# Kernel optimization log

Measured on AMD Instinct MI355X. Metric: run time of the kernel, lower is better.

## Reference

```python
import jax, jax.numpy as jnp
import numpy as np

DIM = 256
NUM_HEADS = 4
HEAD_DIM = DIM // NUM_HEADS


def _linear_params(k, d_in, d_out):
    kw, kb = jax.random.split(k)
    lim = 1.0 / np.sqrt(d_in)
    W = jax.random.uniform(kw, (d_out, d_in), jnp.float32, -lim, lim)
    b = jax.random.uniform(kb, (d_out,), jnp.float32, -lim, lim)
    return W, b


def setup_inputs() -> dict:
    key = jax.random.key(0)
    ks = jax.random.split(key, 10)
    B, Nq, Nkv = 8, 4096, 256
    inp = {
        'node_emb': jax.random.normal(ks[0], (B, Nq, DIM), jnp.float32),
        'cluster_emb': jax.random.normal(ks[1], (B, Nkv, DIM), jnp.float32),
        'clustering_weights': jax.random.normal(ks[2], (B, Nq, Nkv), jnp.float32),
        'ln_q_g': jnp.ones((DIM,), jnp.float32), 'ln_q_b': jnp.zeros((DIM,), jnp.float32),
        'ln_kv_g': jnp.ones((DIM,), jnp.float32), 'ln_kv_b': jnp.zeros((DIM,), jnp.float32),
        'ln_out_g': jnp.ones((DIM,), jnp.float32), 'ln_out_b': jnp.zeros((DIM,), jnp.float32),
    }
    for name, k in [('q', ks[3]), ('k', ks[4]), ('v', ks[5]), ('o', ks[6])]:
        W, b = _linear_params(k, DIM, DIM)
        inp[f'W_{name}'], inp[f'b_{name}'] = W, b
    W1, b1 = _linear_params(ks[7], DIM, DIM)
    W2, b2 = _linear_params(ks[8], DIM, DIM)
    inp.update(W_m1=W1, b_m1=b1, W_m2=W2, b_m2=b2)
    return inp


def _layer_norm(x, g, b, eps=1e-5):
    mu = jnp.mean(x, axis=-1, keepdims=True)
    var = jnp.var(x, axis=-1, keepdims=True)
    return (x - mu) * jax.lax.rsqrt(var + eps) * g + b


def reference(node_emb, cluster_emb, clustering_weights,
              ln_q_g, ln_q_b, ln_kv_g, ln_kv_b, ln_out_g, ln_out_b,
              W_q, b_q, W_k, b_k, W_v, b_v, W_o, b_o,
              W_m1, b_m1, W_m2, b_m2):
    B, Nq, D = node_emb.shape
    Nkv = cluster_emb.shape[1]
    q_in = _layer_norm(node_emb, ln_q_g, ln_q_b)
    kv_in = _layer_norm(cluster_emb, ln_kv_g, ln_kv_b)
    # projections -> [B, H, N, hd]
    Q = (q_in @ W_q.T + b_q).reshape(B, Nq, NUM_HEADS, HEAD_DIM).transpose(0, 2, 1, 3)
    K = (kv_in @ W_k.T + b_k).reshape(B, Nkv, NUM_HEADS, HEAD_DIM).transpose(0, 2, 1, 3)
    V = (kv_in @ W_v.T + b_v).reshape(B, Nkv, NUM_HEADS, HEAD_DIM).transpose(0, 2, 1, 3)
    scores = jnp.einsum('bhqd,bhkd->bhqk', Q, K) / np.sqrt(HEAD_DIM)
    scores = scores + clustering_weights[:, None, :, :]
    attn = jax.nn.softmax(scores, axis=-1)
    ctx = jnp.einsum('bhqk,bhkd->bhqd', attn, V)
    ctx = ctx.transpose(0, 2, 1, 3).reshape(B, Nq, D)
    attn_out = ctx @ W_o.T + b_o
    x = node_emb + attn_out
    h = _layer_norm(x, ln_out_g, ln_out_b)
    h = jax.nn.gelu(h @ W_m1.T + b_m1, approximate=False) @ W_m2.T + b_m2
    out = x + h
    attn_matrix = attn.mean(axis=1)
    return out, attn_matrix
```

## Files before the change

kernel.cpp:

```cpp
#include <hip/hip_runtime.h>
#include <math.h>

typedef __attribute__((ext_vector_type(8))) short short8;
typedef __attribute__((ext_vector_type(4))) float f32x4;
typedef __attribute__((ext_vector_type(2))) unsigned int u32x2;

#define AS1 __attribute__((address_space(1)))
#define AS3 __attribute__((address_space(3)))

__device__ __forceinline__ float b2f(short s){
  return __uint_as_float(((unsigned int)(unsigned short)s) << 16);
}
__device__ __forceinline__ short f2b(float f){
  unsigned int u = __float_as_uint(f);
  u = (u + 0x7fffu + ((u >> 16) & 1u)) >> 16;
  return (short)u;
}
__device__ __forceinline__ unsigned pk2(float lo, float hi){
  return ((unsigned)(unsigned short)f2b(hi) << 16) | (unsigned)(unsigned short)f2b(lo);
}
__device__ __forceinline__ float ulo(unsigned u){ return __uint_as_float(u << 16); }
__device__ __forceinline__ float uhi(unsigned u){ return __uint_as_float(u & 0xffff0000u); }

__global__ __launch_bounds__(256) void cvt_w(
    const float* __restrict__ s0, const float* __restrict__ s1,
    const float* __restrict__ s2, const float* __restrict__ s3,
    const float* __restrict__ s4, const float* __restrict__ s5,
    short* __restrict__ dst, short* __restrict__ dstS)
{
  const float* srcs[6] = {s0, s1, s2, s3, s4, s5};
  int i = blockIdx.x * 256 + threadIdx.x;
  int mat = i >> 16, rc = i & 65535;
  short v = f2b(srcs[mat][rc]);
  dst[i] = v;
  if (mat >= 3){
    int row = rc >> 8, col = rc & 255;
    int d2 = (mat - 3) * 65536 + ((col >> 5) << 13) + (row << 5)
           + (((col >> 3) & 3) << 3) + (col & 7);
    dstS[d2] = v;
  }
}

__global__ __launch_bounds__(256) void ln_k(
    const float* __restrict__ x, const float* __restrict__ g,
    const float* __restrict__ bta, short* __restrict__ y)
{
  const int row = blockIdx.x, t = threadIdx.x;
  const size_t base = (size_t)row * 256;
  float v = x[base + t];
  float s1 = v, s2 = v * v;
  #pragma unroll
  for (int off = 32; off; off >>= 1){ s1 += __shfl_down(s1, off); s2 += __shfl_down(s2, off); }
  __shared__ float a1[4], a2[4];
  __shared__ float mu_s, rs_s;
  if ((t & 63) == 0){ a1[t >> 6] = s1; a2[t >> 6] = s2; }
  __syncthreads();
  if (t == 0){
    float S1 = a1[0] + a1[1] + a1[2] + a1[3];
    float S2 = a2[0] + a2[1] + a2[2] + a2[3];
    float mu = S1 * 0.00390625f;
    float var = S2 * 0.00390625f - mu * mu;
    mu_s = mu; rs_s = rsqrtf(var + 1e-5f);
  }
  __syncthreads();
  y[base + t] = f2b((v - mu_s) * rs_s * g[t] + bta[t]);
}

template<int OT, int LNA>
__global__ __launch_bounds__(256, 2) void gemmW(
    const short* __restrict__ A, const float* __restrict__ Af,
    const short* __restrict__ W, const float* __restrict__ bias,
    short* __restrict__ outB,
    const float* __restrict__ lnag, const float* __restrict__ lnab)
{
  __shared__ short As[64][264];
  __shared__ short Ws[2][256][40];
  const int tid = threadIdx.x;
  const int m0 = blockIdx.x << 6;
  const int w = tid >> 6, lane = tid & 63;
  const int l15 = lane & 15, g = lane >> 4;

  if (LNA){
    const int row = tid >> 2, c0 = (tid & 3) << 6;
    float vv[64];
    const float* src = &Af[(size_t)(m0 + row) * 256 + c0];
    #pragma unroll
    for (int i = 0; i < 16; ++i) *(f32x4*)&vv[4 * i] = *(const f32x4*)&src[4 * i];
    float s1 = 0.f, s2 = 0.f;
    #pragma unroll
    for (int i = 0; i < 64; ++i){ s1 += vv[i]; s2 += vv[i] * vv[i]; }
    s1 += __shfl_xor(s1, 1); s2 += __shfl_xor(s2, 1);
    s1 += __shfl_xor(s1, 2); s2 += __shfl_xor(s2, 2);
    const float mu = s1 * 0.00390625f;
    const float rs = rsqrtf(s2 * 0.00390625f - mu * mu + 1e-5f);
    #pragma unroll
    for (int i = 0; i < 8; ++i){
      f32x4 gv0 = *(const f32x4*)&lnag[c0 + 8 * i];
      f32x4 gv1 = *(const f32x4*)&lnag[c0 + 8 * i + 4];
      f32x4 bv0 = *(const f32x4*)&lnab[c0 + 8 * i];
      f32x4 bv1 = *(const f32x4*)&lnab[c0 + 8 * i + 4];
      short8 o;
      #pragma unroll
      for (int j = 0; j < 4; ++j) o[j] = f2b((vv[8 * i + j] - mu) * rs * gv0[j] + bv0[j]);
      #pragma unroll
      for (int j = 0; j < 4; ++j) o[4 + j] = f2b((vv[8 * i + 4 + j] - mu) * rs * gv1[j] + bv1[j]);
      *(short8*)&As[row][c0 + 8 * i] = o;
    }
  } else {
    #pragma unroll
    for (int it = 0; it < 8; ++it){
      int idx = tid + (it << 8);
      int row = idx >> 5, c = (idx & 31) << 3;
      *(short8*)&As[row][c] = *(const short8*)&A[(size_t)(m0 + row) * 256 + c];
    }
  }
  #pragma unroll
  for (int it = 0; it < 4; ++it){
    int row = (it << 6) + (tid >> 2), c = (tid & 3) << 3;
    *(short8*)&Ws[0][row][c] = *(const short8*)&W[(size_t)row * 256 + c];
  }
  __syncthreads();

  f32x4 acc[16];
  #pragma unroll
  for (int nt = 0; nt < 16; ++nt) acc[nt] = {0.f, 0.f, 0.f, 0.f};

  int cur = 0;
  for (int s = 0; s < 8; ++s){
    const int k0 = s << 5;
    short8 wreg[4];
    if (s < 7){
      #pragma unroll
      for (int it = 0; it < 4; ++it)
        wreg[it] = *(const short8*)&W[(size_t)((it << 6) + (tid >> 2)) * 256 + k0 + 32 + ((tid & 3) << 3)];
    }
    short8 af = *(const short8*)&As[(w << 4) + l15][k0 + (g << 3)];
    #pragma unroll
    for (int nt = 0; nt < 16; ++nt){
      short8 bf = *(const short8*)&Ws[cur][(nt << 4) + l15][g << 3];
      acc[nt] = __builtin_amdgcn_mfma_f32_16x16x32_bf16(af, bf, acc[nt], 0, 0, 0);
    }
    if (s < 7){
      #pragma unroll
      for (int it = 0; it < 4; ++it)
        *(short8*)&Ws[cur ^ 1][(it << 6) + (tid >> 2)][(tid & 3) << 3] = wreg[it];
    }
    __syncthreads();
    cur ^= 1;
  }

  const int row_l = (w << 4) + (g << 2);
  #pragma unroll
  for (int nt = 0; nt < 16; ++nt){
    const int col = (nt << 4) + l15;
    const float bv = bias[col];
    #pragma unroll
    for (int r = 0; r < 4; ++r){
      const int m = m0 + row_l + r;
      float v = acc[nt][r] + bv;
      if (OT == 1){
        const int b_ = m >> 8, kvr = m & 255;
        const int knt = kvr >> 4, kl = kvr & 15;
        const int h = col >> 6, half = (col >> 5) & 1, kg = (col >> 3) & 3, kj = col & 7;
        outB[(((((size_t)(b_ * 4 + h) * 16 + knt) * 2 + half) * 4 + kg) * 16 + kl) * 8 + kj] = f2b(v);
      }
      if (OT == 2){
        const int b_ = m >> 8, kvj = m & 255;
        const int jp = (kvj & ~31) | (((kvj >> 2) & 3) << 3) | (((kvj >> 4) & 1) << 2) | (kvj & 3);
        const int h = col >> 6, dp = col & 63;
        const int kk = jp >> 5, vg = (jp >> 3) & 3, vj = jp & 7;
        const int vn2 = dp >> 4, vl = dp & 15;
        outB[(((((size_t)(b_ * 4 + h) * 8 + kk) * 4 + vn2) * 4 + vg) * 16 + vl) * 8 + vj] = f2b(v);
      }
      if (OT == 4){
        outB[((((size_t)blockIdx.x * 8 + (col >> 5)) * 4 + w) * 64
              + (((col >> 3) & 3) << 4) + (g << 2) + r) * 8 + (col & 7)] = f2b(v);
      }
    }
  }
}

__global__ __launch_bounds__(256, 2) void attn_k(
    const short* __restrict__ Qf, const short* __restrict__ Kf,
    const short* __restrict__ Vf, const float* __restrict__ cw,
    short* __restrict__ ctx, float* __restrict__ am_out)
{
  extern __shared__ __align__(16) short smem[];
  short* Kl = smem;
  short* Vl = smem + 16384;
  const int b = blockIdx.y;
  const int q0 = blockIdx.x << 6;
  const int tid = threadIdx.x;
  const int w = tid >> 6, lane = tid & 63;
  const int l15 = lane & 15, g = lane >> 4;
  const size_t qw = (size_t)b * 4096 + q0 + (w << 4);
  const size_t qblk = qw >> 4;
  const size_t tileQ = qblk >> 2;
  const int wQ = (int)(qblk & 3);
  const size_t tileC = (size_t)b * 64 + blockIdx.x;

#define STG(dst_, src_) do{ _Pragma("unroll")                                        \
  for (int it_ = 0; it_ < 8; ++it_){ int c_ = (it_ << 8) + tid;                      \
    __builtin_amdgcn_global_load_lds((const AS1 void*)((src_) + (c_ << 3)),          \
                                     (AS3 void*)((dst_) + (c_ << 3)), 16, 0, 0); } }while(0)

  STG(Kl, Kf + ((size_t)(b * 4) << 14));

  unsigned cwp[16][2];
  f32x4 am[16];
  {
    char* reg = (char*)smem + 32768 + (w << 13);
    #pragma unroll
    for (int j = 0; j < 16; ++j){
      f32x4 v = *(const f32x4*)&cw[(qw + j) * 256 + (lane << 2)];
      u32x2 d = { pk2(v[0], v[1]), pk2(v[2], v[3]) };
      unsigned off = ((j << 9) + (lane << 3)) ^ ((j & 7) << 4);
      *(u32x2*)(reg + off) = d;
    }
    __syncthreads();
    #pragma unroll
    for (int nt = 0; nt < 16; ++nt){
      unsigned base = ((l15 << 9) + (nt << 5) + (g << 3)) ^ ((l15 & 7) << 4);
      cwp[nt][0] = *(const unsigned*)(reg + base);
      cwp[nt][1] = *(const unsigned*)(reg + base + 4);
      am[nt] = {0.f, 0.f, 0.f, 0.f};
    }
    __syncthreads();
  }

  for (int h = 0; h < 4; ++h){
    STG(Vl, Vf + ((size_t)(b * 4 + h) << 14));
    short8 qf0 = *(const short8*)&Qf[(((tileQ * 8 + (h << 1)) * 4 + wQ) * 64 + lane) * 8];
    short8 qf1 = *(const short8*)&Qf[(((tileQ * 8 + (h << 1) + 1) * 4 + wQ) * 64 + lane) * 8];

    f32x4 acc[16];
    #pragma unroll
    for (int nt = 0; nt < 16; ++nt) acc[nt] = {0.f, 0.f, 0.f, 0.f};
    __builtin_amdgcn_s_setprio(1);
    #pragma unroll
    for (int nt = 0; nt < 16; ++nt){
      short8 kf0 = *(const short8*)&Kl[(nt << 10) + (lane << 3)];
      acc[nt] = __builtin_amdgcn_mfma_f32_16x16x32_bf16(kf0, qf0, acc[nt], 0, 0, 0);
      short8 kf1 = *(const short8*)&Kl[(nt << 10) + 512 + (lane << 3)];
      acc[nt] = __builtin_amdgcn_mfma_f32_16x16x32_bf16(kf1, qf1, acc[nt], 0, 0, 0);
    }
    __builtin_amdgcn_s_setprio(0);
    __syncthreads();
    if (h < 3) STG(Kl, Kf + ((size_t)(b * 4 + h + 1) << 14));

    float mx = -3.4e38f;
    #pragma unroll
    for (int nt = 0; nt < 16; ++nt){
      float c0 = __uint_as_float(cwp[nt][0] << 16);
      float c1 = __uint_as_float(cwp[nt][0] & 0xffff0000u);
      float c2 = __uint_as_float(cwp[nt][1] << 16);
      float c3 = __uint_as_float(cwp[nt][1] & 0xffff0000u);
      acc[nt][0] = acc[nt][0] * 0.125f + c0;
      acc[nt][1] = acc[nt][1] * 0.125f + c1;
      acc[nt][2] = acc[nt][2] * 0.125f + c2;
      acc[nt][3] = acc[nt][3] * 0.125f + c3;
      mx = fmaxf(mx, fmaxf(fmaxf(acc[nt][0], acc[nt][1]), fmaxf(acc[nt][2], acc[nt][3])));
    }
    mx = fmaxf(mx, __shfl_xor(mx, 16));
    mx = fmaxf(mx, __shfl_xor(mx, 32));
    float sm = 0.f;
    #pragma unroll
    for (int nt = 0; nt < 16; ++nt){
      #pragma unroll
      for (int r = 0; r < 4; ++r){
        float e = __expf(acc[nt][r] - mx);
        acc[nt][r] = e; sm += e;
      }
    }
    sm += __shfl_xor(sm, 16);
    sm += __shfl_xor(sm, 32);
    float inv = 1.f / sm;
    #pragma unroll
    for (int nt = 0; nt < 16; ++nt){
      #pragma unroll
      for (int r = 0; r < 4; ++r){
        float p = acc[nt][r] * inv;
        acc[nt][r] = p;
        am[nt][r] += 0.25f * p;
      }
    }
    f32x4 oc[4] = {{0,0,0,0},{0,0,0,0},{0,0,0,0},{0,0,0,0}};
    __builtin_amdgcn_s_setprio(1);
    #pragma unroll
    for (int kk = 0; kk < 8; ++kk){
      union { short8 s; unsigned u[4]; } pa;
      pa.u[0] = pk2(acc[2 * kk][0],     acc[2 * kk][1]);
      pa.u[1] = pk2(acc[2 * kk][2],     acc[2 * kk][3]);
      pa.u[2] = pk2(acc[2 * kk + 1][0], acc[2 * kk + 1][1]);
      pa.u[3] = pk2(acc[2 * kk + 1][2], acc[2 * kk + 1][3]);
      #pragma unroll
      for (int n2 = 0; n2 < 4; ++n2){
        short8 vb = *(const short8*)&Vl[(((kk << 2) + n2) << 9) + (lane << 3)];
        oc[n2] = __builtin_amdgcn_mfma_f32_16x16x32_bf16(pa.s, vb, oc[n2], 0, 0, 0);
      }
    }
    __builtin_amdgcn_s_setprio(0);
    #pragma unroll
    for (int n2 = 0; n2 < 4; ++n2){
      const int sctx = (h << 1) + (n2 >> 1);
      const int gctx = ((n2 & 1) << 1) + (l15 >> 3);
      const int j = l15 & 7;
      #pragma unroll
      for (int r = 0; r < 4; ++r)
        ctx[(((tileC * 8 + sctx) * 4 + w) * 64 + (gctx << 4) + (g << 2) + r) * 8 + j]
            = f2b(oc[n2][r]);
    }
    __syncthreads();
  }

  {
    char* reg = (char*)smem + (w << 14);
    #pragma unroll
    for (int nt = 0; nt < 16; ++nt){
      unsigned off = ((l15 << 10) + (nt << 6) + (g << 4)) ^ ((l15 & 7) << 4);
      *(f32x4*)(reg + off) = am[nt];
    }
    __syncthreads();
    #pragma unroll
    for (int i2 = 0; i2 < 16; ++i2){
      unsigned fb = (tid << 4) + (i2 << 12);
      unsigned rowin = (fb >> 10) & 15;
      f32x4 v = *(const f32x4*)((char*)smem + (fb ^ ((rowin & 7) << 4)));
      unsigned row = fb >> 10;
      *(f32x4*)&am_out[((size_t)b * 4096 + q0 + row) * 256 + ((fb & 1023) >> 2)] = v;
    }
  }
#undef STG
}

__global__ __launch_bounds__(512, 4) void tail_k(
    const short* __restrict__ ctxaf, const short* __restrict__ Wst,
    const float* __restrict__ b_o, const float* __restrict__ b_m1,
    const float* __restrict__ b_m2, const float* __restrict__ node,
    const float* __restrict__ lng, const float* __restrict__ lnb,
    float* __restrict__ outF)
{
  extern __shared__ __align__(16) short lds[];
  short* Ws0 = lds + 16896;
  short* Ws1 = Ws0 + 8192;
  float* part = (float*)(lds + 33280);
  const int tid = threadIdx.x;
  const int tile = blockIdx.x;
  const int m0 = tile << 6;
  const int w = tid >> 6, lane = tid & 63;
  const int l15 = lane & 15, g = lane >> 4;
  const int wm = w >> 1, wn = w & 1;
  const int row_l = (wm << 4) + (g << 2);
  const int colb = wn << 7;

#define ASW(row_, col_) (*(short*)((char*)lds + (row_) * 528 + \
    (((col_) ^ ((((row_) >> 2) & 3) << 3)) << 1)))
#define ASR8(row_, boff_) (*(const short8*)((char*)lds + (row_) * 528 + \
    ((boff_) ^ ((((row_) >> 2) & 3) << 4))))
#define STGW(dst_, wmat_, s_) do{ _Pragma("unroll")                                  \
  for (int it_ = 0; it_ < 2; ++it_){ int c_ = (it_ << 9) + tid;                      \
    __builtin_amdgcn_global_load_lds(                                               \
        (const AS1 void*)((wmat_) + ((size_t)(s_) << 13) + (c_ << 3)),              \
        (AS3 void*)((dst_) + (c_ << 3)), 16, 0, 0); } }while(0)
#define KLOOP(WMAT, AF_EXPR)                                                         \
  do{ int cur = 0;                                                                   \
    _Pragma("unroll")                                                                \
    for (int s = 0; s < 8; ++s){                                                     \
      short* rbuf = cur ? Ws1 : Ws0;                                                 \
      short* sbuf = cur ? Ws0 : Ws1;                                                 \
      if (s < 7){ STGW(sbuf, WMAT, s + 1);                                           \
        asm volatile("s_waitcnt vmcnt(2)" ::: "memory");                             \
      } else {                                                                       \
        asm volatile("s_waitcnt vmcnt(0)" ::: "memory");                             \
      }                                                                              \
      __builtin_amdgcn_s_barrier();                                                  \
      __builtin_amdgcn_sched_barrier(0);                                             \
      const short8 af = (AF_EXPR);                                                   \
      __builtin_amdgcn_s_setprio(1);                                                 \
      _Pragma("unroll")                                                              \
      for (int ntl = 0; ntl < 8; ++ntl){                                             \
        short8 bf = *(const short8*)&rbuf[(((wn << 3) + ntl) * 16 + l15) * 32 + (g << 3)]; \
        acc[ntl] = __builtin_amdgcn_mfma_f32_16x16x32_bf16(af, bf, acc[ntl], 0, 0, 0); \
      }                                                                              \
      __builtin_amdgcn_s_setprio(0);                                                 \
      __builtin_amdgcn_s_barrier();                                                  \
      __builtin_amdgcn_sched_barrier(0);                                             \
      cur ^= 1;                                                                      \
    } }while(0)

  f32x4 acc[8];

  STGW(Ws0, Wst, 0);
  short8 afr[8];
  #pragma unroll
  for (int s = 0; s < 8; ++s)
    afr[s] = *(const short8*)&ctxaf[((((size_t)tile << 3) + s) * 4 + wm) * 512 + (lane << 3)];
  #pragma unroll
  for (int ntl = 0; ntl < 8; ++ntl) acc[ntl] = {0.f, 0.f, 0.f, 0.f};
  KLOOP(Wst, afr[s]);

  unsigned xvp[8][2];
  #pragma unroll
  for (int ntl = 0; ntl < 8; ++ntl){
    const int col = colb + (ntl << 4) + l15;
    const float bv = b_o[col];
    float x0 = acc[ntl][0] + bv + node[(size_t)(m0 + row_l + 0) * 256 + col];
    float x1 = acc[ntl][1] + bv + node[(size_t)(m0 + row_l + 1) * 256 + col];
    float x2 = acc[ntl][2] + bv + node[(size_t)(m0 + row_l + 2) * 256 + col];
    float x3 = acc[ntl][3] + bv + node[(size_t)(m0 + row_l + 3) * 256 + col];
    xvp[ntl][0] = pk2(x0, x1);
    xvp[ntl][1] = pk2(x2, x3);
  }
  #pragma unroll
  for (int r = 0; r < 4; ++r){
    float s1 = 0.f, s2 = 0.f;
    #pragma unroll
    for (int ntl = 0; ntl < 8; ++ntl){
      float v = (r == 0) ? ulo(xvp[ntl][0]) : (r == 1) ? uhi(xvp[ntl][0])
              : (r == 2) ? ulo(xvp[ntl][1]) : uhi(xvp[ntl][1]);
      s1 += v; s2 += v * v;
    }
    #pragma unroll
    for (int off = 1; off < 16; off <<= 1){ s1 += __shfl_xor(s1, off); s2 += __shfl_xor(s2, off); }
    if (l15 == 0){
      part[((row_l + r) * 2 + wn) * 2]     = s1;
      part[((row_l + r) * 2 + wn) * 2 + 1] = s2;
    }
  }
  __syncthreads();
  #pragma unroll
  for (int r = 0; r < 4; ++r){
    const int row = row_l + r;
    const float S1 = part[(row * 2) * 2]     + part[(row * 2 + 1) * 2];
    const float S2 = part[(row * 2) * 2 + 1] + part[(row * 2 + 1) * 2 + 1];
    const float mu = S1 * 0.00390625f;
    const float rs = rsqrtf(S2 * 0.00390625f - mu * mu + 1e-5f);
    #pragma unroll
    for (int ntl = 0; ntl < 8; ++ntl){
      const int col = colb + (ntl << 4) + l15;
      float v = (r == 0) ? ulo(xvp[ntl][0]) : (r == 1) ? uhi(xvp[ntl][0])
              : (r == 2) ? ulo(xvp[ntl][1]) : uhi(xvp[ntl][1]);
      ASW(row, col) = f2b((v - mu) * rs * lng[col] + lnb[col]);
    }
  }

  {
    const short* Wm1 = Wst + 65536;
    STGW(Ws0, Wm1, 0);
    __syncthreads();
    #pragma unroll
    for (int ntl = 0; ntl < 8; ++ntl) acc[ntl] = {0.f, 0.f, 0.f, 0.f};
    KLOOP(Wm1, ASR8((wm << 4) + l15, (s << 6) + (g << 4)));
  }
  #pragma unroll
  for (int ntl = 0; ntl < 8; ++ntl){
    const int col = colb + (ntl << 4) + l15;
    const float bv = b_m1[col];
    #pragma unroll
    for (int r = 0; r < 4; ++r){
      float v = acc[ntl][r] + bv;
      v = 0.5f * v * (1.0f + erff(v * 0.70710678118f));
      ASW(row_l + r, col) = f2b(v);
    }
  }

  {
    const short* Wm2 = Wst + 131072;
    STGW(Ws0, Wm2, 0);
    __syncthreads();
    #pragma unroll
    for (int ntl = 0; ntl < 8; ++ntl) acc[ntl] = {0.f, 0.f, 0.f, 0.f};
    KLOOP(Wm2, ASR8((wm << 4) + l15, (s << 6) + (g << 4)));
  }
  #pragma unroll
  for (int ntl = 0; ntl < 8; ++ntl){
    const int col = colb + (ntl << 4) + l15;
    const float bv = b_m2[col];
    #pragma unroll
    for (int r = 0; r < 4; ++r){
      float xr = (r == 0) ? ulo(xvp[ntl][0]) : (r == 1) ? uhi(xvp[ntl][0])
               : (r == 2) ? ulo(xvp[ntl][1]) : uhi(xvp[ntl][1]);
      outF[(size_t)(m0 + row_l + r) * 256 + col] = acc[ntl][r] + bv + xr;
    }
  }
#undef ASW
#undef ASR8
#undef STGW
#undef KLOOP
}

extern "C" void kernel_launch(void* const* d_in, const int* in_sizes, int n_in,
                              void* d_out, int out_size, void* d_ws, size_t ws_size,
                              hipStream_t stream)
{
  const float* node_emb = (const float*)d_in[0];
  const float* cluster  = (const float*)d_in[1];
  const float* cw       = (const float*)d_in[2];
  const float* ln_q_g   = (const float*)d_in[3];
  const float* ln_q_b   = (const float*)d_in[4];
  const float* ln_kv_g  = (const float*)d_in[5];
  const float* ln_kv_b  = (const float*)d_in[6];
  const float* ln_o_g   = (const float*)d_in[7];
  const float* ln_o_b   = (const float*)d_in[8];
  const float* W_q  = (const float*)d_in[9];  const float* b_q  = (const float*)d_in[10];
  const float* W_k  = (const float*)d_in[11]; const float* b_k  = (const float*)d_in[12];
  const float* W_v  = (const float*)d_in[13]; const float* b_v  = (const float*)d_in[14];
  const float* W_o  = (const float*)d_in[15]; const float* b_o  = (const float*)d_in[16];
  const float* W_m1 = (const float*)d_in[17]; const float* b_m1 = (const float*)d_in[18];
  const float* W_m2 = (const float*)d_in[19]; const float* b_m2 = (const float*)d_in[20];

  char* ws = (char*)d_ws;
  short* Wbf   = (short*)ws;
  short* Wst   = (short*)(ws + 786432);
  short* bufA  = (short*)(ws + 1179648);
  short* bufB  = (short*)(ws + 1179648 + 16777216);
  short* kvin  = (short*)(ws + 1179648 + 2 * 16777216);
  short* kfrag = (short*)(ws + 1179648 + 2 * 16777216 + 1048576);
  short* vfrag = (short*)(ws + 1179648 + 2 * 16777216 + 2 * 1048576);

  float* outF = (float*)d_out;
  float* amof = (float*)d_out + 8388608;

  hipFuncSetAttribute((const void*)attn_k, hipFuncAttributeMaxDynamicSharedMemorySize, 65536);
  hipFuncSetAttribute((const void*)tail_k, hipFuncAttributeMaxDynamicSharedMemorySize, 67584);

  cvt_w<<<1536, 256, 0, stream>>>(W_q, W_k, W_v, W_o, W_m1, W_m2, Wbf, Wst);
  ln_k<<<2048, 256, 0, stream>>>(cluster, ln_kv_g, ln_kv_b, kvin);
  gemmW<4,1><<<512, 256, 0, stream>>>(nullptr, node_emb, Wbf, b_q, bufB, ln_q_g, ln_q_b);
  gemmW<1,0><<<32, 256, 0, stream>>>(kvin, nullptr, Wbf + 65536,  b_k, kfrag, nullptr, nullptr);
  gemmW<2,0><<<32, 256, 0, stream>>>(kvin, nullptr, Wbf + 131072, b_v, vfrag, nullptr, nullptr);
  attn_k<<<dim3(64, 8), 256, 65536, stream>>>(bufB, kfrag, vfrag, cw, bufA, amof);
  tail_k<<<512, 512, 67584, stream>>>(bufA, Wst, b_o, b_m1, b_m2,
      node_emb, ln_o_g, ln_o_b, outF);
}
```

Measured before the change: 117.0 us.

## Fuse KV layernorm with K/V projections and rewrite Q projection GEMM

Drops the separate cluster layernorm kernel and merges the K and V projection GEMMs into one kernel that normalizes in-register and reuses the A tile for both weight matrices. The Q projection becomes a new 512-thread kernel with an XOR-swizzled A tile, direct global-to-LDS weight loads from a pre-tiled W_q copy, and double buffering with explicit waitcnt, barrier and priority control. cvt_w now also writes the tiled W_q layout. This cuts kernel launches and intermediate traffic, and it adds complexity in the new layouts and the hand-scheduled synchronisation.

Result: no change. 115.5 us (-1.3%).

```diff
diff --git a/kernel.cpp b/kernel.cpp
--- a/kernel.cpp
+++ b/kernel.cpp
@@ -33,45 +33,21 @@
   int mat = i >> 16, rc = i & 65535;
   short v = f2b(srcs[mat][rc]);
   dst[i] = v;
-  if (mat >= 3){
+  int slot = (mat >= 3) ? (mat - 3) : (mat == 0 ? 3 : -1);
+  if (slot >= 0){
     int row = rc >> 8, col = rc & 255;
-    int d2 = (mat - 3) * 65536 + ((col >> 5) << 13) + (row << 5)
+    int d2 = slot * 65536 + ((col >> 5) << 13) + (row << 5)
            + (((col >> 3) & 3) << 3) + (col & 7);
     dstS[d2] = v;
   }
 }
 
-__global__ __launch_bounds__(256) void ln_k(
-    const float* __restrict__ x, const float* __restrict__ g,
-    const float* __restrict__ bta, short* __restrict__ y)
-{
-  const int row = blockIdx.x, t = threadIdx.x;
-  const size_t base = (size_t)row * 256;
-  float v = x[base + t];
-  float s1 = v, s2 = v * v;
-  #pragma unroll
-  for (int off = 32; off; off >>= 1){ s1 += __shfl_down(s1, off); s2 += __shfl_down(s2, off); }
-  __shared__ float a1[4], a2[4];
-  __shared__ float mu_s, rs_s;
-  if ((t & 63) == 0){ a1[t >> 6] = s1; a2[t >> 6] = s2; }
-  __syncthreads();
-  if (t == 0){
-    float S1 = a1[0] + a1[1] + a1[2] + a1[3];
-    float S2 = a2[0] + a2[1] + a2[2] + a2[3];
-    float mu = S1 * 0.00390625f;
-    float var = S2 * 0.00390625f - mu * mu;
-    mu_s = mu; rs_s = rsqrtf(var + 1e-5f);
-  }
-  __syncthreads();
-  y[base + t] = f2b((v - mu_s) * rs_s * g[t] + bta[t]);
-}
-
-template<int OT, int LNA>
-__global__ __launch_bounds__(256, 2) void gemmW(
-    const short* __restrict__ A, const float* __restrict__ Af,
-    const short* __restrict__ W, const float* __restrict__ bias,
-    short* __restrict__ outB,
-    const float* __restrict__ lnag, const float* __restrict__ lnab)
+__global__ __launch_bounds__(256, 2) void kv_k(
+    const float* __restrict__ cluster,
+    const short* __restrict__ Wk, const short* __restrict__ Wv,
+    const float* __restrict__ b_k, const float* __restrict__ b_v,
+    const float* __restrict__ lng, const float* __restrict__ lnb,
+    short* __restrict__ kfrag, short* __restrict__ vfrag)
 {
   __shared__ short As[64][264];
   __shared__ short Ws[2][256][40];
@@ -80,10 +56,10 @@
   const int w = tid >> 6, lane = tid & 63;
   const int l15 = lane & 15, g = lane >> 4;
 
-  if (LNA){
+  {
     const int row = tid >> 2, c0 = (tid & 3) << 6;
     float vv[64];
-    const float* src = &Af[(size_t)(m0 + row) * 256 + c0];
+    const float* src = &cluster[(size_t)(m0 + row) * 256 + c0];
     #pragma unroll
     for (int i = 0; i < 16; ++i) *(f32x4*)&vv[4 * i] = *(const f32x4*)&src[4 * i];
     float s1 = 0.f, s2 = 0.f;
@@ -95,10 +71,10 @@
     const float rs = rsqrtf(s2 * 0.00390625f - mu * mu + 1e-5f);
     #pragma unroll
     for (int i = 0; i < 8; ++i){
-      f32x4 gv0 = *(const f32x4*)&lnag[c0 + 8 * i];
-      f32x4 gv1 = *(const f32x4*)&lnag[c0 + 8 * i + 4];
-      f32x4 bv0 = *(const f32x4*)&lnab[c0 + 8 * i];
-      f32x4 bv1 = *(const f32x4*)&lnab[c0 + 8 * i + 4];
+      f32x4 gv0 = *(const f32x4*)&lng[c0 + 8 * i];
+      f32x4 gv1 = *(const f32x4*)&lng[c0 + 8 * i + 4];
+      f32x4 bv0 = *(const f32x4*)&lnb[c0 + 8 * i];
+      f32x4 bv1 = *(const f32x4*)&lnb[c0 + 8 * i + 4];
       short8 o;
       #pragma unroll
       for (int j = 0; j < 4; ++j) o[j] = f2b((vv[8 * i + j] - mu) * rs * gv0[j] + bv0[j]);
@@ -106,78 +82,182 @@
       for (int j = 0; j < 4; ++j) o[4 + j] = f2b((vv[8 * i + 4 + j] - mu) * rs * gv1[j] + bv1[j]);
       *(short8*)&As[row][c0 + 8 * i] = o;
     }
-  } else {
-    #pragma unroll
-    for (int it = 0; it < 8; ++it){
-      int idx = tid + (it << 8);
-      int row = idx >> 5, c = (idx & 31) << 3;
-      *(short8*)&As[row][c] = *(const short8*)&A[(size_t)(m0 + row) * 256 + c];
-    }
-  }
-  #pragma unroll
-  for (int it = 0; it < 4; ++it){
-    int row = (it << 6) + (tid >> 2), c = (tid & 3) << 3;
-    *(short8*)&Ws[0][row][c] = *(const short8*)&W[(size_t)row * 256 + c];
-  }
-  __syncthreads();
+  }
 
   f32x4 acc[16];
-  #pragma unroll
-  for (int nt = 0; nt < 16; ++nt) acc[nt] = {0.f, 0.f, 0.f, 0.f};
-
-  int cur = 0;
-  for (int s = 0; s < 8; ++s){
-    const int k0 = s << 5;
-    short8 wreg[4];
-    if (s < 7){
-      #pragma unroll
-      for (int it = 0; it < 4; ++it)
-        wreg[it] = *(const short8*)&W[(size_t)((it << 6) + (tid >> 2)) * 256 + k0 + 32 + ((tid & 3) << 3)];
-    }
-    short8 af = *(const short8*)&As[(w << 4) + l15][k0 + (g << 3)];
-    #pragma unroll
-    for (int nt = 0; nt < 16; ++nt){
-      short8 bf = *(const short8*)&Ws[cur][(nt << 4) + l15][g << 3];
-      acc[nt] = __builtin_amdgcn_mfma_f32_16x16x32_bf16(af, bf, acc[nt], 0, 0, 0);
-    }
-    if (s < 7){
-      #pragma unroll
-      for (int it = 0; it < 4; ++it)
-        *(short8*)&Ws[cur ^ 1][(it << 6) + (tid >> 2)][(tid & 3) << 3] = wreg[it];
-    }
-    __syncthreads();
-    cur ^= 1;
-  }
-
   const int row_l = (w << 4) + (g << 2);
+
+#define KV_LOOP(WMAT)                                                                 \
+  do{                                                                                 \
+    _Pragma("unroll")                                                                 \
+    for (int it = 0; it < 4; ++it){                                                   \
+      int row = (it << 6) + (tid >> 2), c = (tid & 3) << 3;                           \
+      *(short8*)&Ws[0][row][c] = *(const short8*)&(WMAT)[(size_t)row * 256 + c];      \
+    }                                                                                 \
+    __syncthreads();                                                                  \
+    _Pragma("unroll")                                                                 \
+    for (int nt = 0; nt < 16; ++nt) acc[nt] = (f32x4){0.f, 0.f, 0.f, 0.f};            \
+    int cur = 0;                                                                      \
+    for (int s = 0; s < 8; ++s){                                                      \
+      const int k0 = s << 5;                                                          \
+      short8 wreg[4];                                                                 \
+      if (s < 7){                                                                     \
+        _Pragma("unroll")                                                             \
+        for (int it = 0; it < 4; ++it)                                                \
+          wreg[it] = *(const short8*)&(WMAT)[(size_t)((it << 6) + (tid >> 2)) * 256 + k0 + 32 + ((tid & 3) << 3)]; \
+      }                                                                               \
+      short8 af = *(const short8*)&As[(w << 4) + l15][k0 + (g << 3)];                 \
+      _Pragma("unroll")                                                               \
+      for (int nt = 0; nt < 16; ++nt){                                                \
+        short8 bf = *(const short8*)&Ws[cur][(nt << 4) + l15][g << 3];                \
+        acc[nt] = __builtin_amdgcn_mfma_f32_16x16x32_bf16(af, bf, acc[nt], 0, 0, 0);  \
+      }                                                                               \
+      if (s < 7){                                                                     \
+        _Pragma("unroll")                                                             \
+        for (int it = 0; it < 4; ++it)                                                \
+          *(short8*)&Ws[cur ^ 1][(it << 6) + (tid >> 2)][(tid & 3) << 3] = wreg[it];  \
+      }                                                                               \
+      __syncthreads();                                                                \
+      cur ^= 1;                                                                       \
+    }                                                                                 \
+  }while(0)
+
+  KV_LOOP(Wk);
   #pragma unroll
   for (int nt = 0; nt < 16; ++nt){
     const int col = (nt << 4) + l15;
-    const float bv = bias[col];
+    const float bv = b_k[col];
     #pragma unroll
     for (int r = 0; r < 4; ++r){
       const int m = m0 + row_l + r;
       float v = acc[nt][r] + bv;
-      if (OT == 1){
-        const int b_ = m >> 8, kvr = m & 255;
-        const int knt = kvr >> 4, kl = kvr & 15;
-        const int h = col >> 6, half = (col >> 5) & 1, kg = (col >> 3) & 3, kj = col & 7;
-        outB[(((((size_t)(b_ * 4 + h) * 16 + knt) * 2 + half) * 4 + kg) * 16 + kl) * 8 + kj] = f2b(v);
+      const int b_ = m >> 8, kvr = m & 255;
+      const int knt = kvr >> 4, kl = kvr & 15;
+      const int h = col >> 6, half = (col >> 5) & 1, kg = (col >> 3) & 3, kj = col & 7;
+      kfrag[(((((size_t)(b_ * 4 + h) * 16 + knt) * 2 + half) * 4 + kg) * 16 + kl) * 8 + kj] = f2b(v);
+    }
+  }
+  KV_LOOP(Wv);
+  #pragma unroll
+  for (int nt = 0; nt < 16; ++nt){
+    const int col = (nt << 4) + l15;
+    const float bv = b_v[col];
+    #pragma unroll
+    for (int r = 0; r < 4; ++r){
+      const int m = m0 + row_l + r;
+      float v = acc[nt][r] + bv;
+      const int b_ = m >> 8, kvj = m & 255;
+      const int jp = (kvj & ~31) | (((kvj >> 2) & 3) << 3) | (((kvj >> 4) & 1) << 2) | (kvj & 3);
+      const int h = col >> 6, dp = col & 63;
+      const int kk = jp >> 5, vg = (jp >> 3) & 3, vj = jp & 7;
+      const int vn2 = dp >> 4, vl = dp & 15;
+      vfrag[(((((size_t)(b_ * 4 + h) * 8 + kk) * 4 + vn2) * 4 + vg) * 16 + vl) * 8 + vj] = f2b(v);
+    }
+  }
+#undef KV_LOOP
+}
+
+__global__ __launch_bounds__(512, 4) void qgemm_k(
+    const float* __restrict__ node, const short* __restrict__ Wq,
+    const float* __restrict__ bias,
+    const float* __restrict__ lng, const float* __restrict__ lnb,
+    short* __restrict__ outB)
+{
+  extern __shared__ __align__(16) short lds[];
+  short* Ws0 = lds + 16896;
+  short* Ws1 = Ws0 + 8192;
+  const int tid = threadIdx.x;
+  const int tile = blockIdx.x;
+  const int m0 = tile << 6;
+  const int w = tid >> 6, lane = tid & 63;
+  const int l15 = lane & 15, g = lane >> 4;
+  const int wm = w >> 1, wn = w & 1;
+  const int row_l = (wm << 4) + (g << 2);
+  const int colb = wn << 7;
+
+#define ASW8(row_, col0_) (*(short8*)((char*)lds + (row_) * 528 + \
+    (((col0_) << 1) ^ ((((row_) >> 2) & 3) << 4))))
+#define ASR8(row_, boff_) (*(const short8*)((char*)lds + (row_) * 528 + \
+    ((boff_) ^ ((((row_) >> 2) & 3) << 4))))
+#define STGW(dst_, wmat_, s_) do{ _Pragma("unroll")                                  \
+  for (int it_ = 0; it_ < 2; ++it_){ int c_ = (it_ << 9) + tid;                      \
+    __builtin_amdgcn_global_load_lds(                                               \
+        (const AS1 void*)((wmat_) + ((size_t)(s_) << 13) + (c_ << 3)),              \
+        (AS3 void*)((dst_) + (c_ << 3)), 16, 0, 0); } }while(0)
+
+  {
+    const int row = tid >> 3, c0 = (tid & 7) << 5;
+    float vv[32];
+    const float* src = &node[(size_t)(m0 + row) * 256 + c0];
+    #pragma unroll
+    for (int i = 0; i < 8; ++i) *(f32x4*)&vv[4 * i] = *(const f32x4*)&src[4 * i];
+    float s1 = 0.f, s2 = 0.f;
+    #pragma unroll
+    for (int i = 0; i < 32; ++i){ s1 += vv[i]; s2 += vv[i] * vv[i]; }
+    s1 += __shfl_xor(s1, 1); s2 += __shfl_xor(s2, 1);
+    s1 += __shfl_xor(s1, 2); s2 += __shfl_xor(s2, 2);
+    s1 += __shfl_xor(s1, 4); s2 += __shfl_xor(s2, 4);
+    const float mu = s1 * 0.00390625f;
+    const float rs = rsqrtf(s2 * 0.00390625f - mu * mu + 1e-5f);
+    #pragma unroll
+    for (int i = 0; i < 4; ++i){
+      const int col0 = c0 + 8 * i;
+      f32x4 g0 = *(const f32x4*)&lng[col0], g1 = *(const f32x4*)&lng[col0 + 4];
+      f32x4 b0 = *(const f32x4*)&lnb[col0], b1 = *(const f32x4*)&lnb[col0 + 4];
+      short8 o;
+      #pragma unroll
+      for (int j = 0; j < 4; ++j) o[j] = f2b((vv[8 * i + j] - mu) * rs * g0[j] + b0[j]);
+      #pragma unroll
+      for (int j = 0; j < 4; ++j) o[4 + j] = f2b((vv[8 * i + 4 + j] - mu) * rs * g1[j] + b1[j]);
+      ASW8(row, col0) = o;
+    }
+  }
+  STGW(Ws0, Wq, 0);
+  __syncthreads();
+
+  f32x4 acc[8];
+  #pragma unroll
+  for (int ntl = 0; ntl < 8; ++ntl) acc[ntl] = {0.f, 0.f, 0.f, 0.f};
+  {
+    int cur = 0;
+    #pragma unroll
+    for (int s = 0; s < 8; ++s){
+      short* rbuf = cur ? Ws1 : Ws0;
+      short* sbuf = cur ? Ws0 : Ws1;
+      if (s < 7){ STGW(sbuf, Wq, s + 1);
+        asm volatile("s_waitcnt vmcnt(2)" ::: "memory");
+      } else {
+        asm volatile("s_waitcnt vmcnt(0)" ::: "memory");
       }
-      if (OT == 2){
-        const int b_ = m >> 8, kvj = m & 255;
-        const int jp = (kvj & ~31) | (((kvj >> 2) & 3) << 3) | (((kvj >> 4) & 1) << 2) | (kvj & 3);
-        const int h = col >> 6, dp = col & 63;
-        const int kk = jp >> 5, vg = (jp >> 3) & 3, vj = jp & 7;
-        const int vn2 = dp >> 4, vl = dp & 15;
-        outB[(((((size_t)(b_ * 4 + h) * 8 + kk) * 4 + vn2) * 4 + vg) * 16 + vl) * 8 + vj] = f2b(v);
+      __builtin_amdgcn_s_barrier();
+      __builtin_amdgcn_sched_barrier(0);
+      const short8 af = ASR8((wm << 4) + l15, (s << 6) + (g << 4));
+      __builtin_amdgcn_s_setprio(1);
+      #pragma unroll
+      for (int ntl = 0; ntl < 8; ++ntl){
+        short8 bf = *(const short8*)&rbuf[(((wn << 3) + ntl) * 16 + l15) * 32 + (g << 3)];
+        acc[ntl] = __builtin_amdgcn_mfma_f32_16x16x32_bf16(af, bf, acc[ntl], 0, 0, 0);
       }
-      if (OT == 4){
-        outB[((((size_t)blockIdx.x * 8 + (col >> 5)) * 4 + w) * 64
-              + (((col >> 3) & 3) << 4) + (g << 2) + r) * 8 + (col & 7)] = f2b(v);
-      }
-    }
-  }
+      __builtin_amdgcn_s_setprio(0);
+      __builtin_amdgcn_s_barrier();
+      __builtin_amdgcn_sched_barrier(0);
+      cur ^= 1;
+    }
+  }
+  #pragma unroll
+  for (int ntl = 0; ntl < 8; ++ntl){
+    const int col = colb + (ntl << 4) + l15;
+    const float bv = bias[col];
+    #pragma unroll
+    for (int r = 0; r < 4; ++r){
+      float v = acc[ntl][r] + bv;
+      outB[((((size_t)tile * 8 + (col >> 5)) * 4 + wm) * 64
+            + (((col >> 3) & 3) << 4) + (g << 2) + r) * 8 + (col & 7)] = f2b(v);
+    }
+  }
+#undef ASW8
+#undef ASR8
+#undef STGW
 }
 
 __global__ __launch_bounds__(256, 2) void attn_k(
@@ -512,23 +592,23 @@
   char* ws = (char*)d_ws;
   short* Wbf   = (short*)ws;
   short* Wst   = (short*)(ws + 786432);
-  short* bufA  = (short*)(ws + 1179648);
-  short* bufB  = (short*)(ws + 1179648 + 16777216);
-  short* kvin  = (short*)(ws + 1179648 + 2 * 16777216);
-  short* kfrag = (short*)(ws + 1179648 + 2 * 16777216 + 1048576);
-  short* vfrag = (short*)(ws + 1179648 + 2 * 16777216 + 2 * 1048576);
+  short* bufA  = (short*)(ws + 1310720);
+  short* bufB  = (short*)(ws + 1310720 + 16777216);
+  short* kfrag = (short*)(ws + 1310720 + 2 * 16777216);
+  short* vfrag = (short*)(ws + 1310720 + 2 * 16777216 + 1048576);
 
   float* outF = (float*)d_out;
   float* amof = (float*)d_out + 8388608;
 
-  hipFuncSetAttribute((const void*)attn_k, hipFuncAttributeMaxDynamicSharedMemorySize, 65536);
-  hipFuncSetAttribute((const void*)tail_k, hipFuncAttributeMaxDynamicSharedMemorySize, 67584);
+  hipFuncSetAttribute((const void*)attn_k,  hipFuncAttributeMaxDynamicSharedMemorySize, 65536);
+  hipFuncSetAttribute((const void*)tail_k,  hipFuncAttributeMaxDynamicSharedMemorySize, 67584);
+  hipFuncSetAttribute((const void*)qgemm_k, hipFuncAttributeMaxDynamicSharedMemorySize, 66560);
 
   cvt_w<<<1536, 256, 0, stream>>>(W_q, W_k, W_v, W_o, W_m1, W_m2, Wbf, Wst);
-  ln_k<<<2048, 256, 0, stream>>>(cluster, ln_kv_g, ln_kv_b, kvin);
-  gemmW<4,1><<<512, 256, 0, stream>>>(nullptr, node_emb, Wbf, b_q, bufB, ln_q_g, ln_q_b);
-  gemmW<1,0><<<32, 256, 0, stream>>>(kvin, nullptr, Wbf + 65536,  b_k, kfrag, nullptr, nullptr);
-  gemmW<2,0><<<32, 256, 0, stream>>>(kvin, nullptr, Wbf + 131072, b_v, vfrag, nullptr, nullptr);
+  kv_k<<<32, 256, 0, stream>>>(cluster, Wbf + 65536, Wbf + 131072,
+      b_k, b_v, ln_kv_g, ln_kv_b, kfrag, vfrag);
+  qgemm_k<<<512, 512, 66560, stream>>>(node_emb, Wst + 196608, b_q,
+      ln_q_g, ln_q_b, bufB);
   attn_k<<<dim3(64, 8), 256, 65536, stream>>>(bufB, kfrag, vfrag, cw, bufA, amof);
   tail_k<<<512, 512, 67584, stream>>>(bufA, Wst, b_o, b_m1, b_m2,
       node_emb, ln_o_g, ln_o_b, outF);
```
